# Kernel optimization log

Measured on AMD Instinct MI355X. Metric: run time of the kernel, lower is better.

The kernel has to match this reference:

```python
import jax, jax.numpy as jnp
import numpy as np

B, C, D, H, W = 8, 1, 160, 160, 160
SPATIAL_AXES = (2, 3, 4)  # axial, coronal, sagittal map to dims D, H, W


def setup_inputs() -> dict:
    key = jax.random.key(0)
    k1, _ = jax.random.split(key)
    x = jax.random.normal(k1, (B, C, D, H, W), dtype=jnp.float32)
    log_sigma = jnp.zeros((3,), dtype=jnp.float32)  # log(initial_sigma=1.0)
    return {"x": x, "log_sigma": log_sigma}


def reference(x, log_sigma):
    # For each spatial axis: adjacent-slice diff, squared distance summed over
    # channel + remaining spatial dims (per batch, per slice-pair), RBF kernel,
    # then -mean over (batch, slice-pairs). Equivalent to the original
    # sum_i(-mean_b(k_i)) / (n_slices - 1) since mean is linear.
    sigma = jnp.exp(log_sigma)
    total = jnp.float32(0.0)
    for i, ax in enumerate(SPATIAL_AXES):
        d = jnp.diff(x, axis=ax)  # [B, C, ...] with S-1 along ax
        reduce_dims = tuple(a for a in range(5) if a not in (0, ax))
        sq = jnp.sum(d * d, axis=reduce_dims)  # [B, S-1]
        k = jnp.exp(-sq / (2.0 * sigma[i] ** 2))
        total = total + (-jnp.mean(k))
    return total / jnp.float32(len(SPATIAL_AXES))
```

## Files before the change

kernel.cpp:

```cpp
#include <hip/hip_runtime.h>


constexpr int Wd = 160;
constexpr int SLICE = 160 * 160;
constexpr long BSTRIDE = 160L * 25600;
constexpr int NB = 8;
constexpr int NPAIR = 159;
constexpr int WS_FLOATS = 3 * NB * NPAIR;

__global__ void zero_ws_kernel(float* __restrict__ ws) {
    int i = blockIdx.x * 256 + threadIdx.x;
    if (i < WS_FLOATS) ws[i] = 0.f;
}

__global__ __launch_bounds__(320) void diff3_kernel(const float* __restrict__ x,
                                                    float* __restrict__ ws) {
    __shared__ float accD[10];
    __shared__ float accH[16];
    __shared__ float accW[160];

    const int t = threadIdx.x;
    const int bid = blockIdx.x;
    const int b = bid / 160;
    const int rem = bid % 160;
    const int s = rem / 10;
    const int hc = rem % 10;
    const int h0 = hc * 16;
    const int d0 = s * 10;
    const bool lastSeg = (s == 15);

    const int fw = t % 40;
    const int r1 = t / 40;
    const bool hOK2 = !(hc == 9 && r1 == 7);
    const bool sOK = (fw < 39);

    if (t < 10)              accD[t] = 0.f;
    if (t >= 32 && t < 48)   accH[t - 32] = 0.f;
    if (t >= 64 && t < 224)  accW[t - 64] = 0.f;
    __syncthreads();

    const float* rowA = x + (size_t)b * BSTRIDE + (size_t)d0 * SLICE
                          + (size_t)(h0 + r1) * Wd + (size_t)fw * 4;
    const float* rowB = rowA + 8 * Wd;

    float4 v1 = *(const float4*)rowA;
    float4 v2 = *(const float4*)rowB;
    float4 h1 = *(const float4*)(rowA + Wd);
    float4 h2;
    if (hOK2) h2 = *(const float4*)(rowB + Wd);
    float s1 = 0.f, s2 = 0.f;
    if (sOK) { s1 = rowA[4]; s2 = rowB[4]; }

    float4 p1, p2;
    float aH1 = 0.f, aH2 = 0.f;
    float aW0 = 0.f, aW1 = 0.f, aW2 = 0.f, aW3 = 0.f;

    for (int it = 0; it < 10; ++it) {
        const bool hasNext = (it < 9) || !lastSeg;
        const float* nA = rowA + (size_t)(it + 1) * SLICE;
        const float* nB = rowB + (size_t)(it + 1) * SLICE;
        float4 nv1, nv2, nh1, nh2;
        float ns1 = 0.f, ns2 = 0.f;
        if (hasNext) {
            nv1 = *(const float4*)nA;
            nv2 = *(const float4*)nB;
        }
        if (it < 9) {
            nh1 = *(const float4*)(nA + Wd);
            if (hOK2) nh2 = *(const float4*)(nB + Wd);
            if (sOK) { ns1 = nA[4]; ns2 = nB[4]; }
        }

        float dw;
        dw = v1.y - v1.x; aW0 += dw * dw;
        dw = v1.z - v1.y; aW1 += dw * dw;
        dw = v1.w - v1.z; aW2 += dw * dw;
        dw = v2.y - v2.x; aW0 += dw * dw;
        dw = v2.z - v2.y; aW1 += dw * dw;
        dw = v2.w - v2.z; aW2 += dw * dw;
        if (sOK) {
            dw = s1 - v1.w; aW3 += dw * dw;
            dw = s2 - v2.w; aW3 += dw * dw;
        }
        {
            float e0 = h1.x - v1.x, e1 = h1.y - v1.y, e2 = h1.z - v1.z, e3 = h1.w - v1.w;
            aH1 += e0 * e0 + e1 * e1 + e2 * e2 + e3 * e3;
        }
        if (hOK2) {
            float e0 = h2.x - v2.x, e1 = h2.y - v2.y, e2 = h2.z - v2.z, e3 = h2.w - v2.w;
            aH2 += e0 * e0 + e1 * e1 + e2 * e2 + e3 * e3;
        }
        if (it > 0) {
            float dx0 = v1.x - p1.x, dx1 = v1.y - p1.y, dx2 = v1.z - p1.z, dx3 = v1.w - p1.w;
            float dy0 = v2.x - p2.x, dy1 = v2.y - p2.y, dy2 = v2.z - p2.z, dy3 = v2.w - p2.w;
            float dd = dx0*dx0 + dx1*dx1 + dx2*dx2 + dx3*dx3
                     + dy0*dy0 + dy1*dy1 + dy2*dy2 + dy3*dy3;
            for (int off = 32; off > 0; off >>= 1) dd += __shfl_down(dd, off, 64);
            if ((t & 63) == 0) atomicAdd(&accD[it - 1], dd);
        }

        p1 = v1; p2 = v2;
        if (hasNext) { v1 = nv1; v2 = nv2; }
        if (it < 9) {
            h1 = nh1;
            if (hOK2) h2 = nh2;
            if (sOK) { s1 = ns1; s2 = ns2; }
        }
    }

    if (!lastSeg) {
        float dx0 = v1.x - p1.x, dx1 = v1.y - p1.y, dx2 = v1.z - p1.z, dx3 = v1.w - p1.w;
        float dy0 = v2.x - p2.x, dy1 = v2.y - p2.y, dy2 = v2.z - p2.z, dy3 = v2.w - p2.w;
        float dd = dx0*dx0 + dx1*dx1 + dx2*dx2 + dx3*dx3
                 + dy0*dy0 + dy1*dy1 + dy2*dy2 + dy3*dy3;
        for (int off = 32; off > 0; off >>= 1) dd += __shfl_down(dd, off, 64);
        if ((t & 63) == 0) atomicAdd(&accD[9], dd);
    }

    atomicAdd(&accH[r1], aH1);
    atomicAdd(&accH[r1 + 8], aH2);
    atomicAdd(&accW[fw * 4 + 0], aW0);
    atomicAdd(&accW[fw * 4 + 1], aW1);
    atomicAdd(&accW[fw * 4 + 2], aW2);
    if (sOK) atomicAdd(&accW[fw * 4 + 3], aW3);
    __syncthreads();

    float* wsD = ws;
    float* wsH = ws + NB * NPAIR;
    float* wsW = ws + 2 * NB * NPAIR;
    const int nd = lastSeg ? 9 : 10;
    if (t < nd) atomicAdd(&wsD[b * NPAIR + d0 + t], accD[t]);
    if (t >= 32 && t < 48) {
        int r = t - 32;
        if (h0 + r < 159) atomicAdd(&wsH[b * NPAIR + h0 + r], accH[r]);
    }
    if (t >= 64 && t < 64 + 159) {
        int k = t - 64;
        atomicAdd(&wsW[b * NPAIR + k], accW[k]);
    }
}

__global__ __launch_bounds__(256) void finalize_kernel(const float* __restrict__ ws,
                                                       const float* __restrict__ log_sigma,
                                                       float* __restrict__ out) {
    __shared__ float ssum;
    const int t = threadIdx.x;
    if (t == 0) ssum = 0.f;
    __syncthreads();

    const float f0 = -0.5f * expf(-2.f * log_sigma[0]);
    const float f1 = -0.5f * expf(-2.f * log_sigma[1]);
    const float f2 = -0.5f * expf(-2.f * log_sigma[2]);

    float acc = 0.f;
    const int n = NB * NPAIR;
    for (int i = t; i < n; i += 256) acc += expf(ws[i] * f0);
    for (int i = t; i < n; i += 256) acc += expf(ws[n + i] * f1);
    for (int i = t; i < n; i += 256) acc += expf(ws[2 * n + i] * f2);

    for (int off = 32; off > 0; off >>= 1) acc += __shfl_down(acc, off, 64);
    if ((t & 63) == 0) atomicAdd(&ssum, acc);
    __syncthreads();
    if (t == 0) out[0] = -ssum / (float)(3 * NB * NPAIR);
}

extern "C" void kernel_launch(void* const* d_in, const int* in_sizes, int n_in,
                              void* d_out, int out_size, void* d_ws, size_t ws_size,
                              hipStream_t stream) {
    const float* x = (const float*)d_in[0];
    const float* log_sigma = (const float*)d_in[1];
    float* out = (float*)d_out;
    float* ws = (float*)d_ws;

    zero_ws_kernel<<<(WS_FLOATS + 255) / 256, 256, 0, stream>>>(ws);
    diff3_kernel<<<8 * 10 * 16, 320, 0, stream>>>(x, ws);
    finalize_kernel<<<1, 256, 0, stream>>>(ws, log_sigma, out);
}
```

Before: 218.4 us.

## Pair adjacent rows per thread, unroll depth loop, defer depth reductions

Each thread now handles two adjacent H rows instead of rows eight apart, so the H-difference for the first row reuses the second row already in registers. Only one extra halo row load is needed instead of two. The depth loop is fully unrolled and keeps per-slice depth sums in a 10-element register array, with the wave shuffle reductions and shared atomics moved after the loop. This replaces explicit software prefetching with compiler scheduling, which may raise register pressure and expose load latency.

```diff
diff --git a/kernel.cpp b/kernel.cpp
--- a/kernel.cpp
+++ b/kernel.cpp
@@ -11,6 +11,11 @@
 __global__ void zero_ws_kernel(float* __restrict__ ws) {
     int i = blockIdx.x * 256 + threadIdx.x;
     if (i < WS_FLOATS) ws[i] = 0.f;
+}
+
+__device__ __forceinline__ float sq4(const float4& a, const float4& c) {
+    float e0 = a.x - c.x, e1 = a.y - c.y, e2 = a.z - c.z, e3 = a.w - c.w;
+    return e0 * e0 + e1 * e1 + e2 * e2 + e3 * e3;
 }
 
 __global__ __launch_bounds__(320) void diff3_kernel(const float* __restrict__ x,
@@ -30,46 +35,35 @@
     const bool lastSeg = (s == 15);
 
     const int fw = t % 40;
-    const int r1 = t / 40;
-    const bool hOK2 = !(hc == 9 && r1 == 7);
+    const int rp = t / 40;
+    const int r1 = h0 + 2 * rp;
+    const bool hOK = !(hc == 9 && rp == 7);
     const bool sOK = (fw < 39);
 
     if (t < 10)              accD[t] = 0.f;
     if (t >= 32 && t < 48)   accH[t - 32] = 0.f;
     if (t >= 64 && t < 224)  accW[t - 64] = 0.f;
-    __syncthreads();
 
     const float* rowA = x + (size_t)b * BSTRIDE + (size_t)d0 * SLICE
-                          + (size_t)(h0 + r1) * Wd + (size_t)fw * 4;
-    const float* rowB = rowA + 8 * Wd;
+                          + (size_t)r1 * Wd + (size_t)fw * 4;
 
-    float4 v1 = *(const float4*)rowA;
-    float4 v2 = *(const float4*)rowB;
-    float4 h1 = *(const float4*)(rowA + Wd);
-    float4 h2;
-    if (hOK2) h2 = *(const float4*)(rowB + Wd);
-    float s1 = 0.f, s2 = 0.f;
-    if (sOK) { s1 = rowA[4]; s2 = rowB[4]; }
+    float aW0 = 0.f, aW1 = 0.f, aW2 = 0.f, aW3 = 0.f;
+    float aH1 = 0.f, aH2 = 0.f;
+    float aD[10];
+#pragma unroll
+    for (int j = 0; j < 10; ++j) aD[j] = 0.f;
 
-    float4 p1, p2;
-    float aH1 = 0.f, aH2 = 0.f;
-    float aW0 = 0.f, aW1 = 0.f, aW2 = 0.f, aW3 = 0.f;
+    float4 pv1, pv2;
 
+#pragma unroll
     for (int it = 0; it < 10; ++it) {
-        const bool hasNext = (it < 9) || !lastSeg;
-        const float* nA = rowA + (size_t)(it + 1) * SLICE;
-        const float* nB = rowB + (size_t)(it + 1) * SLICE;
-        float4 nv1, nv2, nh1, nh2;
-        float ns1 = 0.f, ns2 = 0.f;
-        if (hasNext) {
-            nv1 = *(const float4*)nA;
-            nv2 = *(const float4*)nB;
-        }
-        if (it < 9) {
-            nh1 = *(const float4*)(nA + Wd);
-            if (hOK2) nh2 = *(const float4*)(nB + Wd);
-            if (sOK) { ns1 = nA[4]; ns2 = nB[4]; }
-        }
+        const float* sp = rowA + (size_t)it * SLICE;
+        const float4 v1 = *(const float4*)sp;
+        const float4 v2 = *(const float4*)(sp + Wd);
+        float4 hv;
+        if (hOK) hv = *(const float4*)(sp + 2 * Wd);
+        float s1 = 0.f, s2 = 0.f;
+        if (sOK) { s1 = sp[4]; s2 = sp[Wd + 4]; }
 
         float dw;
         dw = v1.y - v1.x; aW0 += dw * dw;
@@ -82,47 +76,32 @@
             dw = s1 - v1.w; aW3 += dw * dw;
             dw = s2 - v2.w; aW3 += dw * dw;
         }
-        {
-            float e0 = h1.x - v1.x, e1 = h1.y - v1.y, e2 = h1.z - v1.z, e3 = h1.w - v1.w;
-            aH1 += e0 * e0 + e1 * e1 + e2 * e2 + e3 * e3;
-        }
-        if (hOK2) {
-            float e0 = h2.x - v2.x, e1 = h2.y - v2.y, e2 = h2.z - v2.z, e3 = h2.w - v2.w;
-            aH2 += e0 * e0 + e1 * e1 + e2 * e2 + e3 * e3;
-        }
-        if (it > 0) {
-            float dx0 = v1.x - p1.x, dx1 = v1.y - p1.y, dx2 = v1.z - p1.z, dx3 = v1.w - p1.w;
-            float dy0 = v2.x - p2.x, dy1 = v2.y - p2.y, dy2 = v2.z - p2.z, dy3 = v2.w - p2.w;
-            float dd = dx0*dx0 + dx1*dx1 + dx2*dx2 + dx3*dx3
-                     + dy0*dy0 + dy1*dy1 + dy2*dy2 + dy3*dy3;
-            for (int off = 32; off > 0; off >>= 1) dd += __shfl_down(dd, off, 64);
-            if ((t & 63) == 0) atomicAdd(&accD[it - 1], dd);
-        }
-
-        p1 = v1; p2 = v2;
-        if (hasNext) { v1 = nv1; v2 = nv2; }
-        if (it < 9) {
-            h1 = nh1;
-            if (hOK2) h2 = nh2;
-            if (sOK) { s1 = ns1; s2 = ns2; }
-        }
+        aH1 += sq4(v2, v1);
+        if (hOK) aH2 += sq4(hv, v2);
+        if (it > 0) aD[it - 1] += sq4(v1, pv1) + sq4(v2, pv2);
+        pv1 = v1; pv2 = v2;
+    }
+    if (!lastSeg) {
+        const float* sp = rowA + (size_t)10 * SLICE;
+        const float4 v1 = *(const float4*)sp;
+        const float4 v2 = *(const float4*)(sp + Wd);
+        aD[9] += sq4(v1, pv1) + sq4(v2, pv2);
     }
 
-    if (!lastSeg) {
-        float dx0 = v1.x - p1.x, dx1 = v1.y - p1.y, dx2 = v1.z - p1.z, dx3 = v1.w - p1.w;
-        float dy0 = v2.x - p2.x, dy1 = v2.y - p2.y, dy2 = v2.z - p2.z, dy3 = v2.w - p2.w;
-        float dd = dx0*dx0 + dx1*dx1 + dx2*dx2 + dx3*dx3
-                 + dy0*dy0 + dy1*dy1 + dy2*dy2 + dy3*dy3;
-        for (int off = 32; off > 0; off >>= 1) dd += __shfl_down(dd, off, 64);
-        if ((t & 63) == 0) atomicAdd(&accD[9], dd);
-    }
+    __syncthreads();
 
-    atomicAdd(&accH[r1], aH1);
-    atomicAdd(&accH[r1 + 8], aH2);
+    atomicAdd(&accH[r1 - h0], aH1);
+    if (hOK) atomicAdd(&accH[r1 - h0 + 1], aH2);
     atomicAdd(&accW[fw * 4 + 0], aW0);
     atomicAdd(&accW[fw * 4 + 1], aW1);
     atomicAdd(&accW[fw * 4 + 2], aW2);
     if (sOK) atomicAdd(&accW[fw * 4 + 3], aW3);
+#pragma unroll
+    for (int j = 0; j < 10; ++j) {
+        float dd = aD[j];
+        for (int off = 32; off > 0; off >>= 1) dd += __shfl_down(dd, off, 64);
+        if ((t & 63) == 0) atomicAdd(&accD[j], dd);
+    }
     __syncthreads();
 
     float* wsD = ws;
```

Result: slower. 228.0 us (+4.4%).
